# Kernel tuning notes

Measured on AMD Instinct MI355X. Metric: run time of the kernel, lower is better.

## Reference

```python
import jax, jax.numpy as jnp
import numpy as np


def setup_inputs() -> dict:
    key = jax.random.key(0)
    k1, k2, k3 = jax.random.split(key, 3)
    N, C, W = 64, 64, 4096
    F, WW = 64, 16
    x = jax.random.normal(k1, (N, C, W), dtype=jnp.float32)
    w = jax.random.normal(k2, (F, C, WW), dtype=jnp.float32) * 0.1
    b = jax.random.normal(k3, (F,), dtype=jnp.float32) * 0.1
    return {"x": x, "w": w, "b": b}


def _fft_conv1d(x, w, b):
    # Faithful to Conv1dfftFunction.forward with padding=0, stride=1,
    # index_back=None, out_size=None, use_next_power2=False.
    N, C, W = x.shape
    F, _, WW = w.shape
    out_W = W - WW + 1
    filter_pad = WW - 1                      # pad on each side of x
    dout_pad = out_W - 1
    fft_size = W + 2 * filter_pad + dout_pad  # init_fft_size in the source

    # padded_x: [filter_pad][x][filter_pad + dout_pad]
    px = jnp.pad(x, ((0, 0), (0, 0), (filter_pad, filter_pad + dout_pad)))
    # padded_filter: [filter_pad][w][zeros up to fft_size]
    pw = jnp.pad(w, ((0, 0), (0, 0), (filter_pad, fft_size - WW - filter_pad)))

    xfft = jnp.fft.rfft(px, axis=-1)          # [N, C, half]
    yfft = jnp.fft.rfft(pw, axis=-1)          # [F, C, half]

    # correlate_fft_signals: irfft(xfft * conj(yfft)); the per-sample loop
    # + per-channel sum in the source is a linear op, so sum channels in the
    # frequency domain (equivalent, one irfft instead of N*F*C).
    offt = jnp.einsum('ncf,kcf->nkf', xfft, jnp.conj(yfft))  # [N, F, half]
    out = jnp.fft.irfft(offt, n=fft_size, axis=-1)[..., :out_W]
    return out + b[None, :, None]


def reference(x, w, b):
    return _fft_conv1d(x, w, b)
```

## Files before the change

kernel.cpp:

```cpp
#include <hip/hip_runtime.h>
#include <stdint.h>

typedef __bf16 bf16_t;
typedef bf16_t bf16x8 __attribute__((ext_vector_type(8)));
typedef float f32x4 __attribute__((ext_vector_type(4)));
typedef unsigned short u16;
typedef u16 u16x8 __attribute__((ext_vector_type(8)));

#define N_    64
#define C_    64
#define W_    4096
#define F_    64
#define WW_   16
#define OUTW  4081
#define TT    128
#define TROWS 144
#define CPAD  72
#define KCH   4
#define NCH   8

__device__ __forceinline__ u16 f2bf(float f) {
  union { float f; uint32_t u; } v; v.f = f;
  uint32_t u = v.u;
  u += 0x7fffu + ((u >> 16) & 1u);
  return (u16)(u >> 16);
}

__global__ void pack_w_kernel(const float* __restrict__ w, u16* __restrict__ wp) {
  int idx = blockIdx.x * 256 + threadIdx.x;
  int j     = idx & 7;
  int lane  = (idx >> 3) & 63;
  int fg    = (idx >> 9) & 3;
  int kstep = idx >> 11;
  int f  = fg * 16 + (lane & 15);
  int kg = kstep * 32 + 8 * (lane >> 4) + j;
  int kk = kg >> 6;
  int c  = kg & 63;
  wp[idx] = f2bf(w[(f * C_ + c) * WW_ + kk]);
}

__launch_bounds__(256, 4)
__global__ void conv_kernel(const float* __restrict__ x, const u16* __restrict__ wp,
                            const float* __restrict__ bias, float* __restrict__ out) {
  __shared__ __align__(16) u16 xT[TROWS * CPAD];
  __shared__ __align__(16) u16 wbuf[KCH * 2048];

  const int tid  = threadIdx.x;
  const int lane = tid & 63;
  const int wid  = tid >> 6;
  const int n    = blockIdx.y;
  const int t0   = blockIdx.x * TT;

  const float* xn = x + (size_t)n * C_ * W_;
  for (int task = tid; task < 8 * TROWS; task += 256) {
    int tp = task % TROWS;
    int cg = task / TROWS;
    int tg = t0 + tp; if (tg > W_ - 1) tg = W_ - 1;
    u16x8 v;
#pragma unroll
    for (int i = 0; i < 8; ++i)
      v[i] = f2bf(xn[(size_t)(cg * 8 + i) * W_ + tg]);
    *reinterpret_cast<u16x8*>(&xT[tp * CPAD + cg * 8]) = v;
  }

  f32x4 acc[2][4];
#pragma unroll
  for (int a = 0; a < 2; ++a)
#pragma unroll
    for (int g = 0; g < 4; ++g)
      acc[a][g] = (f32x4){0.f, 0.f, 0.f, 0.f};

  const int rowbase = wid * 32 + (lane & 15);
  const int csub    = 8 * (lane >> 4);

  for (int ch = 0; ch < NCH; ++ch) {
    __syncthreads();
    {
      const u16* src = wp + ch * (KCH * 2048) + wid * 2048 + lane * 8;
      u16* dst = &wbuf[wid * 2048];
#pragma unroll
      for (int i = 0; i < 4; ++i) {
        __builtin_amdgcn_global_load_lds(
            (const __attribute__((address_space(1))) uint32_t*)(src + i * 512),
            (__attribute__((address_space(3))) uint32_t*)(dst + i * 512),
            16, 0, 0);
      }
    }
    __syncthreads();

#pragma unroll
    for (int s = 0; s < KCH; ++s) {
      const int kstep = ch * KCH + s;
      const int kk = kstep >> 1;
      const int cb = (kstep & 1) * 32;
      const u16* arow = &xT[(rowbase + kk) * CPAD + cb + csub];
      bf16x8 a0 = *reinterpret_cast<const bf16x8*>(arow);
      bf16x8 a1 = *reinterpret_cast<const bf16x8*>(arow + 16 * CPAD);
#pragma unroll
      for (int fg = 0; fg < 4; ++fg) {
        bf16x8 bb = *reinterpret_cast<const bf16x8*>(&wbuf[s * 2048 + fg * 512 + lane * 8]);
        acc[0][fg] = __builtin_amdgcn_mfma_f32_16x16x32_bf16(a0, bb, acc[0][fg], 0, 0, 0);
        acc[1][fg] = __builtin_amdgcn_mfma_f32_16x16x32_bf16(a1, bb, acc[1][fg], 0, 0, 0);
      }
    }
  }

  const int fcol = lane & 15;
  const int rq   = (lane >> 4) * 4;
  float bv[4];
#pragma unroll
  for (int fg = 0; fg < 4; ++fg) bv[fg] = bias[fg * 16 + fcol];

#pragma unroll
  for (int rf = 0; rf < 2; ++rf) {
#pragma unroll
    for (int fg = 0; fg < 4; ++fg) {
#pragma unroll
      for (int r = 0; r < 4; ++r) {
        int t = t0 + wid * 32 + rf * 16 + rq + r;
        if (t < OUTW)
          out[((size_t)n * F_ + fg * 16 + fcol) * OUTW + t] = acc[rf][fg][r] + bv[fg];
      }
    }
  }
}

extern "C" void kernel_launch(void* const* d_in, const int* in_sizes, int n_in,
                              void* d_out, int out_size, void* d_ws, size_t ws_size,
                              hipStream_t stream) {
  const float* x = (const float*)d_in[0];
  const float* w = (const float*)d_in[1];
  const float* b = (const float*)d_in[2];
  float* out = (float*)d_out;
  u16* wp = (u16*)d_ws;

  hipLaunchKernelGGL(pack_w_kernel, dim3(256), dim3(256), 0, stream, w, wp);
  dim3 grid((OUTW + TT - 1) / TT, N_);
  hipLaunchKernelGGL(conv_kernel, grid, dim3(256), 0, stream, x, wp, b, out);
}
```

Before: 159.8 us.

## Stage output through LDS for coalesced stores and read weights directly from global

Accumulated results are written to an LDS buffer (aliasing the x tile) and then written out so that consecutive threads store consecutive time indices, replacing the strided per-lane global stores. The weight staging through LDS with global_load_lds and per-chunk barriers is removed, and B fragments are loaded straight from global (L2-resident) memory. This removes the barriers inside the loop and makes stores coalesced, at the cost of more global load latency in the MMA loop.

Result: faster. 152.1 us (-4.8%).

```diff
diff --git a/kernel.cpp b/kernel.cpp
--- a/kernel.cpp
+++ b/kernel.cpp
@@ -16,8 +16,8 @@
 #define TT    128
 #define TROWS 144
 #define CPAD  72
-#define KCH   4
-#define NCH   8
+#define OPAD  65
+#define NKS   32
 
 __device__ __forceinline__ u16 f2bf(float f) {
   union { float f; uint32_t u; } v; v.f = f;
@@ -42,8 +42,9 @@
 __launch_bounds__(256, 4)
 __global__ void conv_kernel(const float* __restrict__ x, const u16* __restrict__ wp,
                             const float* __restrict__ bias, float* __restrict__ out) {
-  __shared__ __align__(16) u16 xT[TROWS * CPAD];
-  __shared__ __align__(16) u16 wbuf[KCH * 2048];
+  __shared__ __align__(16) char smem_raw[TT * OPAD * 4];
+  u16*   xT   = reinterpret_cast<u16*>(smem_raw);
+  float* obuf = reinterpret_cast<float*>(smem_raw);
 
   const int tid  = threadIdx.x;
   const int lane = tid & 63;
@@ -62,6 +63,7 @@
       v[i] = f2bf(xn[(size_t)(cg * 8 + i) * W_ + tg]);
     *reinterpret_cast<u16x8*>(&xT[tp * CPAD + cg * 8]) = v;
   }
+  __syncthreads();
 
   f32x4 acc[2][4];
 #pragma unroll
@@ -72,37 +74,27 @@
 
   const int rowbase = wid * 32 + (lane & 15);
   const int csub    = 8 * (lane >> 4);
+  const u16* wpB    = wp + (size_t)lane * 8;
 
-  for (int ch = 0; ch < NCH; ++ch) {
-    __syncthreads();
-    {
-      const u16* src = wp + ch * (KCH * 2048) + wid * 2048 + lane * 8;
-      u16* dst = &wbuf[wid * 2048];
-#pragma unroll
-      for (int i = 0; i < 4; ++i) {
-        __builtin_amdgcn_global_load_lds(
-            (const __attribute__((address_space(1))) uint32_t*)(src + i * 512),
-            (__attribute__((address_space(3))) uint32_t*)(dst + i * 512),
-            16, 0, 0);
-      }
-    }
-    __syncthreads();
-
-#pragma unroll
-    for (int s = 0; s < KCH; ++s) {
-      const int kstep = ch * KCH + s;
-      const int kk = kstep >> 1;
-      const int cb = (kstep & 1) * 32;
-      const u16* arow = &xT[(rowbase + kk) * CPAD + cb + csub];
-      bf16x8 a0 = *reinterpret_cast<const bf16x8*>(arow);
-      bf16x8 a1 = *reinterpret_cast<const bf16x8*>(arow + 16 * CPAD);
-#pragma unroll
-      for (int fg = 0; fg < 4; ++fg) {
-        bf16x8 bb = *reinterpret_cast<const bf16x8*>(&wbuf[s * 2048 + fg * 512 + lane * 8]);
-        acc[0][fg] = __builtin_amdgcn_mfma_f32_16x16x32_bf16(a0, bb, acc[0][fg], 0, 0, 0);
-        acc[1][fg] = __builtin_amdgcn_mfma_f32_16x16x32_bf16(a1, bb, acc[1][fg], 0, 0, 0);
-      }
-    }
+#pragma unroll 4
+  for (int ks = 0; ks < NKS; ++ks) {
+    const int kk = ks >> 1;
+    const int cb = (ks & 1) << 5;
+    const u16* arow = &xT[(rowbase + kk) * CPAD + cb + csub];
+    bf16x8 a0 = *reinterpret_cast<const bf16x8*>(arow);
+    bf16x8 a1 = *reinterpret_cast<const bf16x8*>(arow + 16 * CPAD);
+    bf16x8 b0 = *reinterpret_cast<const bf16x8*>(wpB + (size_t)(ks * 4 + 0) * 512);
+    bf16x8 b1 = *reinterpret_cast<const bf16x8*>(wpB + (size_t)(ks * 4 + 1) * 512);
+    bf16x8 b2 = *reinterpret_cast<const bf16x8*>(wpB + (size_t)(ks * 4 + 2) * 512);
+    bf16x8 b3 = *reinterpret_cast<const bf16x8*>(wpB + (size_t)(ks * 4 + 3) * 512);
+    acc[0][0] = __builtin_amdgcn_mfma_f32_16x16x32_bf16(a0, b0, acc[0][0], 0, 0, 0);
+    acc[1][0] = __builtin_amdgcn_mfma_f32_16x16x32_bf16(a1, b0, acc[1][0], 0, 0, 0);
+    acc[0][1] = __builtin_amdgcn_mfma_f32_16x16x32_bf16(a0, b1, acc[0][1], 0, 0, 0);
+    acc[1][1] = __builtin_amdgcn_mfma_f32_16x16x32_bf16(a1, b1, acc[1][1], 0, 0, 0);
+    acc[0][2] = __builtin_amdgcn_mfma_f32_16x16x32_bf16(a0, b2, acc[0][2], 0, 0, 0);
+    acc[1][2] = __builtin_amdgcn_mfma_f32_16x16x32_bf16(a1, b2, acc[1][2], 0, 0, 0);
+    acc[0][3] = __builtin_amdgcn_mfma_f32_16x16x32_bf16(a0, b3, acc[0][3], 0, 0, 0);
+    acc[1][3] = __builtin_amdgcn_mfma_f32_16x16x32_bf16(a1, b3, acc[1][3], 0, 0, 0);
   }
 
   const int fcol = lane & 15;
@@ -111,17 +103,24 @@
 #pragma unroll
   for (int fg = 0; fg < 4; ++fg) bv[fg] = bias[fg * 16 + fcol];
 
+  __syncthreads();
 #pragma unroll
-  for (int rf = 0; rf < 2; ++rf) {
+  for (int rf = 0; rf < 2; ++rf)
 #pragma unroll
-    for (int fg = 0; fg < 4; ++fg) {
+    for (int fg = 0; fg < 4; ++fg)
 #pragma unroll
-      for (int r = 0; r < 4; ++r) {
-        int t = t0 + wid * 32 + rf * 16 + rq + r;
-        if (t < OUTW)
-          out[((size_t)n * F_ + fg * 16 + fcol) * OUTW + t] = acc[rf][fg][r] + bv[fg];
-      }
-    }
+      for (int r = 0; r < 4; ++r)
+        obuf[(wid * 32 + rf * 16 + rq + r) * OPAD + fg * 16 + fcol] = acc[rf][fg][r] + bv[fg];
+  __syncthreads();
+
+#pragma unroll
+  for (int i = 0; i < 32; ++i) {
+    int p  = tid + 256 * i;
+    int f  = p >> 7;
+    int tl = p & 127;
+    int t  = t0 + tl;
+    if (t < OUTW)
+      out[((size_t)n * F_ + f) * OUTW + t] = obuf[tl * OPAD + f];
   }
 }
 
```

## Double time tile, swap MFMA operands, stream weights from global with register prefetch

Applied to the files above, without the earlier changes.

Doubles the time tile per block to 256 outputs, so each wave computes a 64x64 output tile with 16 accumulators instead of 8. Weights are no longer staged through LDS in chunks with barriers. They are read directly from global memory into registers with a one-step prefetch, and the weights and input take swapped MFMA operand roles so output stores are coalesced along time. This drops the per-chunk syncs and LDS weight traffic and amortises input staging over more outputs, at the cost of more registers, half as many blocks, and global-latency exposure on the weight loads.

Result: faster. 143.6 us (-10.1%).

```diff
diff --git a/kernel.cpp b/kernel.cpp
--- a/kernel.cpp
+++ b/kernel.cpp
@@ -13,11 +13,10 @@
 #define F_    64
 #define WW_   16
 #define OUTW  4081
-#define TT    128
-#define TROWS 144
+#define TT    256
+#define TROWS 271
 #define CPAD  72
-#define KCH   4
-#define NCH   8
+#define NKS   32
 
 __device__ __forceinline__ u16 f2bf(float f) {
   union { float f; uint32_t u; } v; v.f = f;
@@ -30,20 +29,20 @@
   int idx = blockIdx.x * 256 + threadIdx.x;
   int j     = idx & 7;
   int lane  = (idx >> 3) & 63;
-  int fg    = (idx >> 9) & 3;
+  int m     = (idx >> 9) & 3;
   int kstep = idx >> 11;
-  int f  = fg * 16 + (lane & 15);
+  int f  = m * 16 + (lane & 15);
   int kg = kstep * 32 + 8 * (lane >> 4) + j;
   int kk = kg >> 6;
   int c  = kg & 63;
   wp[idx] = f2bf(w[(f * C_ + c) * WW_ + kk]);
 }
 
-__launch_bounds__(256, 4)
+__attribute__((amdgpu_waves_per_eu(4, 4)))
+__launch_bounds__(256)
 __global__ void conv_kernel(const float* __restrict__ x, const u16* __restrict__ wp,
                             const float* __restrict__ bias, float* __restrict__ out) {
   __shared__ __align__(16) u16 xT[TROWS * CPAD];
-  __shared__ __align__(16) u16 wbuf[KCH * 2048];
 
   const int tid  = threadIdx.x;
   const int lane = tid & 63;
@@ -62,64 +61,77 @@
       v[i] = f2bf(xn[(size_t)(cg * 8 + i) * W_ + tg]);
     *reinterpret_cast<u16x8*>(&xT[tp * CPAD + cg * 8]) = v;
   }
+  __syncthreads();
 
-  f32x4 acc[2][4];
+  f32x4 acc[4][4];
 #pragma unroll
-  for (int a = 0; a < 2; ++a)
+  for (int a = 0; a < 4; ++a)
 #pragma unroll
     for (int g = 0; g < 4; ++g)
       acc[a][g] = (f32x4){0.f, 0.f, 0.f, 0.f};
 
-  const int rowbase = wid * 32 + (lane & 15);
-  const int csub    = 8 * (lane >> 4);
+  const int fr = lane & 15;
+  const int kq = lane >> 4;
+  const u16* wpA = wp + (size_t)lane * 8;
+  const u16* xB  = &xT[(wid * 64 + fr) * CPAD + 8 * kq];
 
-  for (int ch = 0; ch < NCH; ++ch) {
-    __syncthreads();
-    {
-      const u16* src = wp + ch * (KCH * 2048) + wid * 2048 + lane * 8;
-      u16* dst = &wbuf[wid * 2048];
-#pragma unroll
-      for (int i = 0; i < 4; ++i) {
-        __builtin_amdgcn_global_load_lds(
-            (const __attribute__((address_space(1))) uint32_t*)(src + i * 512),
-            (__attribute__((address_space(3))) uint32_t*)(dst + i * 512),
-            16, 0, 0);
-      }
-    }
-    __syncthreads();
+  bf16x8 ca0 = *reinterpret_cast<const bf16x8*>(wpA + 0 * 512);
+  bf16x8 ca1 = *reinterpret_cast<const bf16x8*>(wpA + 1 * 512);
+  bf16x8 ca2 = *reinterpret_cast<const bf16x8*>(wpA + 2 * 512);
+  bf16x8 ca3 = *reinterpret_cast<const bf16x8*>(wpA + 3 * 512);
 
 #pragma unroll
-    for (int s = 0; s < KCH; ++s) {
-      const int kstep = ch * KCH + s;
-      const int kk = kstep >> 1;
-      const int cb = (kstep & 1) * 32;
-      const u16* arow = &xT[(rowbase + kk) * CPAD + cb + csub];
-      bf16x8 a0 = *reinterpret_cast<const bf16x8*>(arow);
-      bf16x8 a1 = *reinterpret_cast<const bf16x8*>(arow + 16 * CPAD);
-#pragma unroll
-      for (int fg = 0; fg < 4; ++fg) {
-        bf16x8 bb = *reinterpret_cast<const bf16x8*>(&wbuf[s * 2048 + fg * 512 + lane * 8]);
-        acc[0][fg] = __builtin_amdgcn_mfma_f32_16x16x32_bf16(a0, bb, acc[0][fg], 0, 0, 0);
-        acc[1][fg] = __builtin_amdgcn_mfma_f32_16x16x32_bf16(a1, bb, acc[1][fg], 0, 0, 0);
-      }
+  for (int ks = 0; ks < NKS; ++ks) {
+    const int kk = ks >> 1;
+    const int cb = (ks & 1) << 5;
+    bf16x8 na0, na1, na2, na3;
+    if (ks < NKS - 1) {
+      na0 = *reinterpret_cast<const bf16x8*>(wpA + (size_t)((ks + 1) * 4 + 0) * 512);
+      na1 = *reinterpret_cast<const bf16x8*>(wpA + (size_t)((ks + 1) * 4 + 1) * 512);
+      na2 = *reinterpret_cast<const bf16x8*>(wpA + (size_t)((ks + 1) * 4 + 2) * 512);
+      na3 = *reinterpret_cast<const bf16x8*>(wpA + (size_t)((ks + 1) * 4 + 3) * 512);
     }
+    bf16x8 b0 = *reinterpret_cast<const bf16x8*>(xB + (kk +  0) * CPAD + cb);
+    bf16x8 b1 = *reinterpret_cast<const bf16x8*>(xB + (kk + 16) * CPAD + cb);
+    bf16x8 b2 = *reinterpret_cast<const bf16x8*>(xB + (kk + 32) * CPAD + cb);
+    bf16x8 b3 = *reinterpret_cast<const bf16x8*>(xB + (kk + 48) * CPAD + cb);
+
+    acc[0][0] = __builtin_amdgcn_mfma_f32_16x16x32_bf16(ca0, b0, acc[0][0], 0, 0, 0);
+    acc[1][0] = __builtin_amdgcn_mfma_f32_16x16x32_bf16(ca1, b0, acc[1][0], 0, 0, 0);
+    acc[2][0] = __builtin_amdgcn_mfma_f32_16x16x32_bf16(ca2, b0, acc[2][0], 0, 0, 0);
+    acc[3][0] = __builtin_amdgcn_mfma_f32_16x16x32_bf16(ca3, b0, acc[3][0], 0, 0, 0);
+    acc[0][1] = __builtin_amdgcn_mfma_f32_16x16x32_bf16(ca0, b1, acc[0][1], 0, 0, 0);
+    acc[1][1] = __builtin_amdgcn_mfma_f32_16x16x32_bf16(ca1, b1, acc[1][1], 0, 0, 0);
+    acc[2][1] = __builtin_amdgcn_mfma_f32_16x16x32_bf16(ca2, b1, acc[2][1], 0, 0, 0);
+    acc[3][1] = __builtin_amdgcn_mfma_f32_16x16x32_bf16(ca3, b1, acc[3][1], 0, 0, 0);
+    acc[0][2] = __builtin_amdgcn_mfma_f32_16x16x32_bf16(ca0, b2, acc[0][2], 0, 0, 0);
+    acc[1][2] = __builtin_amdgcn_mfma_f32_16x16x32_bf16(ca1, b2, acc[1][2], 0, 0, 0);
+    acc[2][2] = __builtin_amdgcn_mfma_f32_16x16x32_bf16(ca2, b2, acc[2][2], 0, 0, 0);
+    acc[3][2] = __builtin_amdgcn_mfma_f32_16x16x32_bf16(ca3, b2, acc[3][2], 0, 0, 0);
+    acc[0][3] = __builtin_amdgcn_mfma_f32_16x16x32_bf16(ca0, b3, acc[0][3], 0, 0, 0);
+    acc[1][3] = __builtin_amdgcn_mfma_f32_16x16x32_bf16(ca1, b3, acc[1][3], 0, 0, 0);
+    acc[2][3] = __builtin_amdgcn_mfma_f32_16x16x32_bf16(ca2, b3, acc[2][3], 0, 0, 0);
+    acc[3][3] = __builtin_amdgcn_mfma_f32_16x16x32_bf16(ca3, b3, acc[3][3], 0, 0, 0);
+
+    ca0 = na0; ca1 = na1; ca2 = na2; ca3 = na3;
   }
 
-  const int fcol = lane & 15;
-  const int rq   = (lane >> 4) * 4;
-  float bv[4];
+  f32x4 bv[4];
 #pragma unroll
-  for (int fg = 0; fg < 4; ++fg) bv[fg] = bias[fg * 16 + fcol];
+  for (int m = 0; m < 4; ++m)
+    bv[m] = *reinterpret_cast<const f32x4*>(bias + m * 16 + kq * 4);
 
 #pragma unroll
-  for (int rf = 0; rf < 2; ++rf) {
+  for (int m = 0; m < 4; ++m) {
 #pragma unroll
-    for (int fg = 0; fg < 4; ++fg) {
+    for (int nf = 0; nf < 4; ++nf) {
+      int t = t0 + wid * 64 + nf * 16 + fr;
+      if (t < OUTW) {
 #pragma unroll
-      for (int r = 0; r < 4; ++r) {
-        int t = t0 + wid * 32 + rf * 16 + rq + r;
-        if (t < OUTW)
-          out[((size_t)n * F_ + fg * 16 + fcol) * OUTW + t] = acc[rf][fg][r] + bv[fg];
+        for (int r = 0; r < 4; ++r) {
+          int f = m * 16 + kq * 4 + r;
+          out[((size_t)n * F_ + f) * OUTW + t] = acc[m][nf][r] + bv[m][r];
+        }
       }
     }
   }
```

## Switch to 32x32x16 MFMA with larger time tile and register-prefetched weights

Applied to the files above, without the earlier changes.

Doubles the time tile per block to 256 and replaces the 16x16x32 MFMA with 32x32x16 MFMA. Filters become the A operand and time the B operand, so output stores are coalesced along time. Weights are no longer staged in LDS via global_load_lds with per-chunk barriers; each wave reads them directly from global/L2 with a software prefetch pipeline, leaving one barrier after the x transpose. This cuts LDS traffic and barriers and improves store coalescing, but it raises register pressure, lowers occupancy hints, and halves the number of blocks.

Result: faster. 135.8 us (-15.0%).

```diff
diff --git a/kernel.cpp b/kernel.cpp
--- a/kernel.cpp
+++ b/kernel.cpp
@@ -4,6 +4,7 @@
 typedef __bf16 bf16_t;
 typedef bf16_t bf16x8 __attribute__((ext_vector_type(8)));
 typedef float f32x4 __attribute__((ext_vector_type(4)));
+typedef float f32x16 __attribute__((ext_vector_type(16)));
 typedef unsigned short u16;
 typedef u16 u16x8 __attribute__((ext_vector_type(8)));
 
@@ -13,11 +14,10 @@
 #define F_    64
 #define WW_   16
 #define OUTW  4081
-#define TT    128
-#define TROWS 144
+#define TT    256
+#define TROWS 271
 #define CPAD  72
-#define KCH   4
-#define NCH   8
+#define NKS   64
 
 __device__ __forceinline__ u16 f2bf(float f) {
   union { float f; uint32_t u; } v; v.f = f;
@@ -28,22 +28,22 @@
 
 __global__ void pack_w_kernel(const float* __restrict__ w, u16* __restrict__ wp) {
   int idx = blockIdx.x * 256 + threadIdx.x;
-  int j     = idx & 7;
-  int lane  = (idx >> 3) & 63;
-  int fg    = (idx >> 9) & 3;
-  int kstep = idx >> 11;
-  int f  = fg * 16 + (lane & 15);
-  int kg = kstep * 32 + 8 * (lane >> 4) + j;
+  int j    = idx & 7;
+  int lane = (idx >> 3) & 63;
+  int m    = (idx >> 9) & 1;
+  int ks   = idx >> 10;
+  int f  = m * 32 + (lane & 31);
+  int kg = ks * 16 + (lane >> 5) * 8 + j;
   int kk = kg >> 6;
   int c  = kg & 63;
   wp[idx] = f2bf(w[(f * C_ + c) * WW_ + kk]);
 }
 
-__launch_bounds__(256, 4)
+__attribute__((amdgpu_waves_per_eu(3, 4)))
+__launch_bounds__(256)
 __global__ void conv_kernel(const float* __restrict__ x, const u16* __restrict__ wp,
                             const float* __restrict__ bias, float* __restrict__ out) {
   __shared__ __align__(16) u16 xT[TROWS * CPAD];
-  __shared__ __align__(16) u16 wbuf[KCH * 2048];
 
   const int tid  = threadIdx.x;
   const int lane = tid & 63;
@@ -62,64 +62,69 @@
       v[i] = f2bf(xn[(size_t)(cg * 8 + i) * W_ + tg]);
     *reinterpret_cast<u16x8*>(&xT[tp * CPAD + cg * 8]) = v;
   }
+  __syncthreads();
 
-  f32x4 acc[2][4];
+  f32x16 acc[2][2];
 #pragma unroll
   for (int a = 0; a < 2; ++a)
 #pragma unroll
-    for (int g = 0; g < 4; ++g)
-      acc[a][g] = (f32x4){0.f, 0.f, 0.f, 0.f};
+    for (int g = 0; g < 2; ++g)
+      acc[a][g] = (f32x16){0.f,0.f,0.f,0.f,0.f,0.f,0.f,0.f,0.f,0.f,0.f,0.f,0.f,0.f,0.f,0.f};
 
-  const int rowbase = wid * 32 + (lane & 15);
-  const int csub    = 8 * (lane >> 4);
+  const int rowt = lane & 31;
+  const int hi   = lane >> 5;
+  const int browt = wid * 64 + rowt;
+  const u16* wpA  = wp + (size_t)lane * 8;
 
-  for (int ch = 0; ch < NCH; ++ch) {
-    __syncthreads();
-    {
-      const u16* src = wp + ch * (KCH * 2048) + wid * 2048 + lane * 8;
-      u16* dst = &wbuf[wid * 2048];
-#pragma unroll
-      for (int i = 0; i < 4; ++i) {
-        __builtin_amdgcn_global_load_lds(
-            (const __attribute__((address_space(1))) uint32_t*)(src + i * 512),
-            (__attribute__((address_space(3))) uint32_t*)(dst + i * 512),
-            16, 0, 0);
-      }
-    }
-    __syncthreads();
+#define LA(ks, m) (*reinterpret_cast<const bf16x8*>(wpA + (size_t)((ks) * 2 + (m)) * 512))
+#define LB(ks, nt) (*reinterpret_cast<const bf16x8*>( \
+      &xT[(browt + (nt) * 32 + ((ks) >> 2)) * CPAD + ((ks) & 3) * 16 + hi * 8]))
+
+  bf16x8 ap[3][2];
+  bf16x8 bp[2][2];
+  ap[0][0] = LA(0, 0); ap[0][1] = LA(0, 1);
+  ap[1][0] = LA(1, 0); ap[1][1] = LA(1, 1);
+  bp[0][0] = LB(0, 0); bp[0][1] = LB(0, 1);
 
 #pragma unroll
-    for (int s = 0; s < KCH; ++s) {
-      const int kstep = ch * KCH + s;
-      const int kk = kstep >> 1;
-      const int cb = (kstep & 1) * 32;
-      const u16* arow = &xT[(rowbase + kk) * CPAD + cb + csub];
-      bf16x8 a0 = *reinterpret_cast<const bf16x8*>(arow);
-      bf16x8 a1 = *reinterpret_cast<const bf16x8*>(arow + 16 * CPAD);
+  for (int ks = 0; ks < NKS; ++ks) {
+    if (ks + 2 < NKS) {
+      ap[(ks + 2) % 3][0] = LA(ks + 2, 0);
+      ap[(ks + 2) % 3][1] = LA(ks + 2, 1);
+    }
+    if (ks + 1 < NKS) {
+      bp[(ks + 1) & 1][0] = LB(ks + 1, 0);
+      bp[(ks + 1) & 1][1] = LB(ks + 1, 1);
+    }
+    acc[0][0] = __builtin_amdgcn_mfma_f32_32x32x16_bf16(ap[ks % 3][0], bp[ks & 1][0], acc[0][0], 0, 0, 0);
+    acc[0][1] = __builtin_amdgcn_mfma_f32_32x32x16_bf16(ap[ks % 3][0], bp[ks & 1][1], acc[0][1], 0, 0, 0);
+    acc[1][0] = __builtin_amdgcn_mfma_f32_32x32x16_bf16(ap[ks % 3][1], bp[ks & 1][0], acc[1][0], 0, 0, 0);
+    acc[1][1] = __builtin_amdgcn_mfma_f32_32x32x16_bf16(ap[ks % 3][1], bp[ks & 1][1], acc[1][1], 0, 0, 0);
+  }
+#undef LA
+#undef LB
+
+  f32x4 bv[2][4];
 #pragma unroll
-      for (int fg = 0; fg < 4; ++fg) {
-        bf16x8 bb = *reinterpret_cast<const bf16x8*>(&wbuf[s * 2048 + fg * 512 + lane * 8]);
-        acc[0][fg] = __builtin_amdgcn_mfma_f32_16x16x32_bf16(a0, bb, acc[0][fg], 0, 0, 0);
-        acc[1][fg] = __builtin_amdgcn_mfma_f32_16x16x32_bf16(a1, bb, acc[1][fg], 0, 0, 0);
-      }
-    }
-  }
-
-  const int fcol = lane & 15;
-  const int rq   = (lane >> 4) * 4;
-  float bv[4];
+  for (int m = 0; m < 2; ++m)
 #pragma unroll
-  for (int fg = 0; fg < 4; ++fg) bv[fg] = bias[fg * 16 + fcol];
+    for (int rq = 0; rq < 4; ++rq)
+      bv[m][rq] = *reinterpret_cast<const f32x4*>(bias + m * 32 + rq * 8 + hi * 4);
 
 #pragma unroll
-  for (int rf = 0; rf < 2; ++rf) {
+  for (int m = 0; m < 2; ++m) {
 #pragma unroll
-    for (int fg = 0; fg < 4; ++fg) {
+    for (int nt = 0; nt < 2; ++nt) {
+      int t = t0 + wid * 64 + nt * 32 + rowt;
+      if (t < OUTW) {
 #pragma unroll
-      for (int r = 0; r < 4; ++r) {
-        int t = t0 + wid * 32 + rf * 16 + rq + r;
-        if (t < OUTW)
-          out[((size_t)n * F_ + fg * 16 + fcol) * OUTW + t] = acc[rf][fg][r] + bv[fg];
+        for (int rq = 0; rq < 4; ++rq) {
+#pragma unroll
+          for (int r2 = 0; r2 < 4; ++r2) {
+            int f = m * 32 + hi * 4 + rq * 8 + r2;
+            out[((size_t)n * F_ + f) * OUTW + t] = acc[m][nt][rq * 4 + r2] + bv[m][rq][r2];
+          }
+        }
       }
     }
   }
```
